# Kernel optimization log

Measured on AMD Instinct MI355X. Metric: run time of the kernel, lower is better.

## Reference

```python
import jax, jax.numpy as jnp
import numpy as np

B, C = 8192, 1000
T_KD = 20.0   # KL_divergence temperature
T_TH = 2.0    # Threshold_weights5 temperature
ALPHA = 0.8   # dynamic weight scale


def setup_inputs() -> dict:
    key = jax.random.key(0)
    ks = jax.random.split(key, 7)
    d = {f"outputs{i+1}": jax.random.normal(ks[i], (B, C), jnp.float32) for i in range(5)}
    d["out_s"] = jax.random.normal(ks[5], (B, C), jnp.float32)
    d["targets"] = jax.random.randint(ks[6], (B,), 0, C)
    return d


def _margin(o, targets):
    # per-sample: top1 - top2 if the target class holds the max logit, else 0
    top2 = jax.lax.top_k(o, 2)[0]                                   # [B, 2]
    tgt = jnp.take_along_axis(o, targets[:, None], axis=1)[:, 0]    # [B]
    return jnp.where(tgt == top2[:, 0], top2[:, 0] - top2[:, 1], jnp.zeros_like(tgt))


def reference(outputs1, outputs2, outputs3, outputs4, outputs5, out_s, targets):
    teachers = jnp.stack([outputs1, outputs2, outputs3, outputs4, outputs5], 0)  # [5,B,C]
    mimic = teachers.mean(0)                                                      # [B,C]
    all6 = jnp.concatenate([teachers, mimic[None]], axis=0)                       # [6,B,C]

    # Threshold_weights5: confidence margins -> softmax over the 6 sources
    margins = jax.vmap(lambda o: _margin(o, targets))(all6)        # [6,B]
    out_threshold = jax.nn.softmax(margins / T_TH, axis=0)         # [6,B]
    max_preds = teachers.max()                                     # scalar

    # Calculate_dynamic_weights for each source
    tgt_logits = jnp.take_along_axis(all6, targets[None, :, None], axis=2)[..., 0]  # [6,B]
    w2 = ALPHA * tgt_logits / max_preds                            # [6,B]
    w1 = 1.0 - w2                                                  # [6,B]

    # CE loss (shared across sources) and KD cross-entropy per source
    log_p_s = jax.nn.log_softmax(out_s, axis=1)
    CE = -jnp.take_along_axis(log_p_s, targets[:, None], axis=1)[:, 0]             # [B]
    log_p_sT = jax.nn.log_softmax(out_s / T_KD, axis=1)                            # [B,C]
    p_t = jax.nn.softmax(all6 / T_KD, axis=2)                                      # [6,B,C]
    KD = -jnp.sum(p_t * log_p_sT[None], axis=2) * (T_KD * T_KD)                    # [6,B]

    loss_src = w1 * CE[None, :] + w2 * KD                          # [6,B]
    return jnp.mean(jnp.sum(out_threshold * loss_src, axis=0))
```

## Files before the change

kernel.cpp:

```cpp
#include <hip/hip_runtime.h>
#include <math.h>

#define NROWS 8192
#define NCOLS 1000
#define TPB   256
#define WPB   4
#define NB    (NROWS / WPB)
#define NSLOT 64
#define NEGF  -1.0e30f


__device__ __forceinline__ unsigned encf(float x) {
    unsigned u = __float_as_uint(x);
    return (u & 0x80000000u) ? ~u : (u | 0x80000000u);
}
__device__ __forceinline__ float decf(unsigned e) {
    unsigned u = (e & 0x80000000u) ? (e ^ 0x80000000u) : ~e;
    return __uint_as_float(u);
}
__device__ __forceinline__ float pick4(const float* a, int k) {
    return k == 0 ? a[0] : (k == 1 ? a[1] : (k == 2 ? a[2] : a[3]));
}

__global__ __launch_bounds__(TPB, 4) void row_kernel(
    const float* __restrict__ p0, const float* __restrict__ p1,
    const float* __restrict__ p2, const float* __restrict__ p3,
    const float* __restrict__ p4, const float* __restrict__ p5,
    const int* __restrict__ targets,
    double* __restrict__ S1, double* __restrict__ S2, unsigned* __restrict__ MX)
{
    const int wave = threadIdx.x >> 6;
    const int l    = threadIdx.x & 63;
    const int row  = blockIdx.x * WPB + wave;

    const int tgt = targets[row];
    const int t4  = tgt >> 2;
    const int lt  = t4 & 63;
    const int qt  = t4 >> 6;
    const int kt  = tgt & 3;

    float m1[6], m2[6], zs[6], ds[6];
    #pragma unroll
    for (int s = 0; s < 6; ++s) { m1[s] = NEGF; m2[s] = NEGF; zs[s] = 0.f; ds[s] = 0.f; }
    float z1 = 0.f, z20 = 0.f;
    float sg[7];
    #pragma unroll
    for (int s = 0; s < 7; ++s) sg[s] = 0.f;

    #pragma unroll 2
    for (int q = 0; q < 4; ++q) {
        const int  c4 = l + (q << 6);
        const bool ok = (c4 < (NCOLS >> 2));
        const size_t base = (size_t)row * NCOLS + ((size_t)c4 << 2);

        float v[7][4];
        if (ok) {
            float4 x0 = *(const float4*)(p0 + base);
            float4 x1 = *(const float4*)(p1 + base);
            float4 x2 = *(const float4*)(p2 + base);
            float4 x3 = *(const float4*)(p3 + base);
            float4 x4 = *(const float4*)(p4 + base);
            float4 x5 = *(const float4*)(p5 + base);
            v[0][0]=x0.x; v[0][1]=x0.y; v[0][2]=x0.z; v[0][3]=x0.w;
            v[1][0]=x1.x; v[1][1]=x1.y; v[1][2]=x1.z; v[1][3]=x1.w;
            v[2][0]=x2.x; v[2][1]=x2.y; v[2][2]=x2.z; v[2][3]=x2.w;
            v[3][0]=x3.x; v[3][1]=x3.y; v[3][2]=x3.z; v[3][3]=x3.w;
            v[4][0]=x4.x; v[4][1]=x4.y; v[4][2]=x4.z; v[4][3]=x4.w;
            v[6][0]=x5.x; v[6][1]=x5.y; v[6][2]=x5.z; v[6][3]=x5.w;
            #pragma unroll
            for (int k = 0; k < 4; ++k)
                v[5][k] = (v[0][k] + v[1][k] + v[2][k] + v[3][k] + v[4][k]) * 0.2f;
        } else {
            #pragma unroll
            for (int s = 0; s < 7; ++s)
                #pragma unroll
                for (int k = 0; k < 4; ++k) v[s][k] = NEGF;
        }

        #pragma unroll
        for (int s = 0; s < 6; ++s) {
            float a = v[s][0], b = v[s][1], c = v[s][2], d = v[s][3];
            float hi1 = fmaxf(a, b), lo1 = fminf(a, b);
            float hi2 = fmaxf(c, d), lo2 = fminf(c, d);
            float q1 = fmaxf(hi1, hi2);
            float q2 = fmaxf(fminf(hi1, hi2), fmaxf(lo1, lo2));
            float nm1 = fmaxf(m1[s], q1);
            float nm2 = fmaxf(fminf(m1[s], q1), fmaxf(m2[s], q2));
            m1[s] = nm1; m2[s] = nm2;
            float zz = 0.f, dot = 0.f;
            #pragma unroll
            for (int k = 0; k < 4; ++k) {
                float e = __expf(v[s][k] * 0.05f);
                zz += e; dot += e * v[6][k];
            }
            zs[s] += zz; ds[s] += dot;
        }
        #pragma unroll
        for (int k = 0; k < 4; ++k) {
            z1  += __expf(v[6][k]);
            z20 += __expf(v[6][k] * 0.05f);
        }
        if (ok && q == qt && l == lt) {
            #pragma unroll
            for (int s = 0; s < 7; ++s) sg[s] = pick4(v[s], kt);
        }
    }

    #pragma unroll
    for (int xm = 1; xm < 64; xm <<= 1) {
        #pragma unroll
        for (int s = 0; s < 6; ++s) {
            float o1 = __shfl_xor(m1[s], xm);
            float o2 = __shfl_xor(m2[s], xm);
            float nm1 = fmaxf(m1[s], o1);
            float nm2 = fmaxf(fminf(m1[s], o1), fmaxf(m2[s], o2));
            m1[s] = nm1; m2[s] = nm2;
            zs[s] += __shfl_xor(zs[s], xm);
            ds[s] += __shfl_xor(ds[s], xm);
        }
        z1  += __shfl_xor(z1, xm);
        z20 += __shfl_xor(z20, xm);
    }
    float sgv[7];
    #pragma unroll
    for (int s = 0; s < 7; ++s) sgv[s] = __shfl(sg[s], lt);

    if (l == 0) {
        const float lse1  = logf(z1);
        const float lse20 = logf(z20);
        const float CE    = lse1 - sgv[6];

        float KD[6], mg[6];
        float mmax = 0.f;
        #pragma unroll
        for (int s = 0; s < 6; ++s) {
            KD[s] = 400.f * lse20 - 20.f * (ds[s] / zs[s]);
            mg[s] = (sgv[s] == m1[s]) ? (m1[s] - m2[s]) : 0.f;
            mmax  = fmaxf(mmax, mg[s]);
        }
        float es[6], se = 0.f;
        #pragma unroll
        for (int s = 0; s < 6; ++s) { es[s] = __expf((mg[s] - mmax) * 0.5f); se += es[s]; }

        double rS2 = 0.0;
        #pragma unroll
        for (int s = 0; s < 6; ++s)
            rS2 += (double)(es[s] / se) * (double)sgv[s] * (double)(KD[s] - CE);

        float tmax = fmaxf(fmaxf(fmaxf(m1[0], m1[1]), fmaxf(m1[2], m1[3])), m1[4]);
        atomicAdd(&S1[row & (NSLOT - 1)], (double)CE);
        atomicAdd(&S2[row & (NSLOT - 1)], rS2);
        atomicMax(&MX[row & (NSLOT - 1)], encf(tmax));
    }
}

__global__ void final_kernel(const double* __restrict__ S1, const double* __restrict__ S2,
                             const unsigned* __restrict__ MX, float* __restrict__ out)
{
    const int tid = threadIdx.x;
    double s1 = S1[tid], s2 = S2[tid];
    unsigned m = MX[tid];
    #pragma unroll
    for (int k = 32; k >= 1; k >>= 1) {
        s1 += __shfl_xor(s1, k);
        s2 += __shfl_xor(s2, k);
        unsigned om = __shfl_xor(m, k);
        m = (om > m) ? om : m;
    }
    if (tid == 0) {
        double maxp = (double)decf(m);
        out[0] = (float)((s1 + (0.8 / maxp) * s2) / (double)NROWS);
    }
}

extern "C" void kernel_launch(void* const* d_in, const int* in_sizes, int n_in,
                              void* d_out, int out_size, void* d_ws, size_t ws_size,
                              hipStream_t stream)
{
    const float* t1 = (const float*)d_in[0];
    const float* t2 = (const float*)d_in[1];
    const float* t3 = (const float*)d_in[2];
    const float* t4 = (const float*)d_in[3];
    const float* t5 = (const float*)d_in[4];
    const float* os = (const float*)d_in[5];
    const int* targets = (const int*)d_in[6];

    double*   S1 = (double*)d_ws;
    double*   S2 = S1 + NSLOT;
    unsigned* MX = (unsigned*)(S2 + NSLOT);

    hipMemsetAsync(d_ws, 0, NSLOT * (8 + 8 + 4), stream);
    row_kernel<<<NB, TPB, 0, stream>>>(t1, t2, t3, t4, t5, os, targets, S1, S2, MX);
    final_kernel<<<1, 64, 0, stream>>>(S1, S2, MX, (float*)d_out);
}
```

Before: 214.3 us.

## Software-pipeline row loads with inline asm double buffering and manual vmcnt waits

Replaces the compiler-scheduled column loop with explicit inline-asm global_load_dwordx4 batches into two register buffers. The next chunk's six loads are issued while the current chunk is processed, with s_waitcnt vmcnt gating each stage. The tail chunk clamps its address and masks padded lanes, so the bounds branch goes away. Launch bounds are relaxed from 4 to 3 waves per SIMD to fit the extra live registers, which trades occupancy for memory-level parallelism inside each wave.

```diff
diff --git a/kernel.cpp b/kernel.cpp
--- a/kernel.cpp
+++ b/kernel.cpp
@@ -9,6 +9,8 @@
 #define NSLOT 64
 #define NEGF  -1.0e30f
 
+typedef float f32x4 __attribute__((ext_vector_type(4)));
+
 
 __device__ __forceinline__ unsigned encf(float x) {
     unsigned u = __float_as_uint(x);
@@ -22,7 +24,78 @@
     return k == 0 ? a[0] : (k == 1 ? a[1] : (k == 2 ? a[2] : a[3]));
 }
 
-__global__ __launch_bounds__(TPB, 4) void row_kernel(
+#define LOAD6(X0,X1,X2,X3,X4,X5, A0,A1,A2,A3,A4,A5)                    \
+    asm volatile("global_load_dwordx4 %0, %6, off\n\t"                 \
+                 "global_load_dwordx4 %1, %7, off\n\t"                 \
+                 "global_load_dwordx4 %2, %8, off\n\t"                 \
+                 "global_load_dwordx4 %3, %9, off\n\t"                 \
+                 "global_load_dwordx4 %4, %10, off\n\t"                \
+                 "global_load_dwordx4 %5, %11, off"                    \
+                 : "=&v"(X0), "=&v"(X1), "=&v"(X2), "=&v"(X3), "=&v"(X4), "=&v"(X5) \
+                 : "v"(A0), "v"(A1), "v"(A2), "v"(A3), "v"(A4), "v"(A5) \
+                 : "memory")
+
+#define WAITVM(Nstr) do {                                              \
+    asm volatile("s_waitcnt vmcnt(" Nstr ")" ::: "memory");            \
+    __builtin_amdgcn_sched_barrier(0);                                 \
+} while (0)
+
+__device__ __forceinline__ void chunk_accum(
+    f32x4 X0, f32x4 X1, f32x4 X2, f32x4 X3, f32x4 X4, f32x4 X5,
+    int q, bool pad, int qt, int lt, int kt, int l,
+    float (&m1)[6], float (&m2)[6], float (&zs)[6], float (&ds)[6],
+    float &z1, float &z20, float (&sg)[7])
+{
+    float v[7][4];
+    #pragma unroll
+    for (int k = 0; k < 4; ++k) {
+        v[0][k] = X0[k]; v[1][k] = X1[k]; v[2][k] = X2[k];
+        v[3][k] = X3[k]; v[4][k] = X4[k]; v[6][k] = X5[k];
+    }
+    if (pad) {
+        #pragma unroll
+        for (int s = 0; s < 7; ++s)
+            #pragma unroll
+            for (int k = 0; k < 4; ++k) v[s][k] = NEGF;
+    }
+    #pragma unroll
+    for (int k = 0; k < 4; ++k)
+        v[5][k] = (v[0][k] + v[1][k] + v[2][k] + v[3][k] + v[4][k]) * 0.2f;
+    if (pad) {
+        #pragma unroll
+        for (int k = 0; k < 4; ++k) v[5][k] = NEGF;
+    }
+
+    #pragma unroll
+    for (int s = 0; s < 6; ++s) {
+        float a = v[s][0], b = v[s][1], c = v[s][2], d = v[s][3];
+        float hi1 = fmaxf(a, b), lo1 = fminf(a, b);
+        float hi2 = fmaxf(c, d), lo2 = fminf(c, d);
+        float q1 = fmaxf(hi1, hi2);
+        float q2 = fmaxf(fminf(hi1, hi2), fmaxf(lo1, lo2));
+        float nm1 = fmaxf(m1[s], q1);
+        float nm2 = fmaxf(fminf(m1[s], q1), fmaxf(m2[s], q2));
+        m1[s] = nm1; m2[s] = nm2;
+        float zz = 0.f, dot = 0.f;
+        #pragma unroll
+        for (int k = 0; k < 4; ++k) {
+            float e = __expf(v[s][k] * 0.05f);
+            zz += e; dot += e * v[6][k];
+        }
+        zs[s] += zz; ds[s] += dot;
+    }
+    #pragma unroll
+    for (int k = 0; k < 4; ++k) {
+        z1  += __expf(v[6][k]);
+        z20 += __expf(v[6][k] * 0.05f);
+    }
+    if (!pad && q == qt && l == lt) {
+        #pragma unroll
+        for (int s = 0; s < 7; ++s) sg[s] = pick4(v[s], kt);
+    }
+}
+
+__global__ __launch_bounds__(TPB, 3) void row_kernel(
     const float* __restrict__ p0, const float* __restrict__ p1,
     const float* __restrict__ p2, const float* __restrict__ p3,
     const float* __restrict__ p4, const float* __restrict__ p5,
@@ -32,12 +105,24 @@
     const int wave = threadIdx.x >> 6;
     const int l    = threadIdx.x & 63;
     const int row  = blockIdx.x * WPB + wave;
+    const size_t rbase = (size_t)row * NCOLS;
 
     const int tgt = targets[row];
     const int t4  = tgt >> 2;
     const int lt  = t4 & 63;
     const int qt  = t4 >> 6;
     const int kt  = tgt & 3;
+    __builtin_amdgcn_sched_barrier(0);
+
+    int c4t = l + 192; if (c4t > 249) c4t = 249;
+    const size_t off0 = rbase + ((size_t)l << 2);
+    const size_t off1 = off0 + 256;
+    const size_t off2 = off0 + 512;
+    const size_t offT = rbase + ((size_t)c4t << 2);
+
+    f32x4 X0,X1,X2,X3,X4,X5, Y0,Y1,Y2,Y3,Y4,Y5;
+    LOAD6(X0,X1,X2,X3,X4,X5, p0+off0, p1+off0, p2+off0, p3+off0, p4+off0, p5+off0);
+    LOAD6(Y0,Y1,Y2,Y3,Y4,Y5, p0+off1, p1+off1, p2+off1, p3+off1, p4+off1, p5+off1);
 
     float m1[6], m2[6], zs[6], ds[6];
     #pragma unroll
@@ -47,64 +132,19 @@
     #pragma unroll
     for (int s = 0; s < 7; ++s) sg[s] = 0.f;
 
-    #pragma unroll 2
-    for (int q = 0; q < 4; ++q) {
-        const int  c4 = l + (q << 6);
-        const bool ok = (c4 < (NCOLS >> 2));
-        const size_t base = (size_t)row * NCOLS + ((size_t)c4 << 2);
-
-        float v[7][4];
-        if (ok) {
-            float4 x0 = *(const float4*)(p0 + base);
-            float4 x1 = *(const float4*)(p1 + base);
-            float4 x2 = *(const float4*)(p2 + base);
-            float4 x3 = *(const float4*)(p3 + base);
-            float4 x4 = *(const float4*)(p4 + base);
-            float4 x5 = *(const float4*)(p5 + base);
-            v[0][0]=x0.x; v[0][1]=x0.y; v[0][2]=x0.z; v[0][3]=x0.w;
-            v[1][0]=x1.x; v[1][1]=x1.y; v[1][2]=x1.z; v[1][3]=x1.w;
-            v[2][0]=x2.x; v[2][1]=x2.y; v[2][2]=x2.z; v[2][3]=x2.w;
-            v[3][0]=x3.x; v[3][1]=x3.y; v[3][2]=x3.z; v[3][3]=x3.w;
-            v[4][0]=x4.x; v[4][1]=x4.y; v[4][2]=x4.z; v[4][3]=x4.w;
-            v[6][0]=x5.x; v[6][1]=x5.y; v[6][2]=x5.z; v[6][3]=x5.w;
-            #pragma unroll
-            for (int k = 0; k < 4; ++k)
-                v[5][k] = (v[0][k] + v[1][k] + v[2][k] + v[3][k] + v[4][k]) * 0.2f;
-        } else {
-            #pragma unroll
-            for (int s = 0; s < 7; ++s)
-                #pragma unroll
-                for (int k = 0; k < 4; ++k) v[s][k] = NEGF;
-        }
-
-        #pragma unroll
-        for (int s = 0; s < 6; ++s) {
-            float a = v[s][0], b = v[s][1], c = v[s][2], d = v[s][3];
-            float hi1 = fmaxf(a, b), lo1 = fminf(a, b);
-            float hi2 = fmaxf(c, d), lo2 = fminf(c, d);
-            float q1 = fmaxf(hi1, hi2);
-            float q2 = fmaxf(fminf(hi1, hi2), fmaxf(lo1, lo2));
-            float nm1 = fmaxf(m1[s], q1);
-            float nm2 = fmaxf(fminf(m1[s], q1), fmaxf(m2[s], q2));
-            m1[s] = nm1; m2[s] = nm2;
-            float zz = 0.f, dot = 0.f;
-            #pragma unroll
-            for (int k = 0; k < 4; ++k) {
-                float e = __expf(v[s][k] * 0.05f);
-                zz += e; dot += e * v[6][k];
-            }
-            zs[s] += zz; ds[s] += dot;
-        }
-        #pragma unroll
-        for (int k = 0; k < 4; ++k) {
-            z1  += __expf(v[6][k]);
-            z20 += __expf(v[6][k] * 0.05f);
-        }
-        if (ok && q == qt && l == lt) {
-            #pragma unroll
-            for (int s = 0; s < 7; ++s) sg[s] = pick4(v[s], kt);
-        }
-    }
+    WAITVM("6");
+    chunk_accum(X0,X1,X2,X3,X4,X5, 0, false, qt,lt,kt,l, m1,m2,zs,ds, z1,z20, sg);
+    LOAD6(X0,X1,X2,X3,X4,X5, p0+off2, p1+off2, p2+off2, p3+off2, p4+off2, p5+off2);
+
+    WAITVM("6");
+    chunk_accum(Y0,Y1,Y2,Y3,Y4,Y5, 1, false, qt,lt,kt,l, m1,m2,zs,ds, z1,z20, sg);
+    LOAD6(Y0,Y1,Y2,Y3,Y4,Y5, p0+offT, p1+offT, p2+offT, p3+offT, p4+offT, p5+offT);
+
+    WAITVM("6");
+    chunk_accum(X0,X1,X2,X3,X4,X5, 2, false, qt,lt,kt,l, m1,m2,zs,ds, z1,z20, sg);
+
+    WAITVM("0");
+    chunk_accum(Y0,Y1,Y2,Y3,Y4,Y5, 3, (l >= 58), qt,lt,kt,l, m1,m2,zs,ds, z1,z20, sg);
 
     #pragma unroll
     for (int xm = 1; xm < 64; xm <<= 1) {
```

Result: no change. 211.1 us (-1.5%).

## Split each row across two waves with a partial-merge kernel pair

Applied to the files above, without the earlier changes.

Each row is now processed by two wavefronts, each covering half of the 1000 columns. All twelve float4 loads are issued up front to raise memory-level parallelism. Per-half partial statistics (top-2, softmax sums, dot products, target gathers) go to a workspace buffer, and a new merge kernel combines them and does the per-row loss. This doubles the wave count and the in-flight loads. The cost is an extra launch, a workspace round-trip and a fallback path when the workspace is too small.

```diff
diff --git a/kernel.cpp b/kernel.cpp
--- a/kernel.cpp
+++ b/kernel.cpp
@@ -3,12 +3,11 @@
 
 #define NROWS 8192
 #define NCOLS 1000
-#define TPB   256
-#define WPB   4
-#define NB    (NROWS / WPB)
 #define NSLOT 64
 #define NEGF  -1.0e30f
-
+#define NHALF (NROWS * 2)
+#define NCOMP 33
+#define WS_NEEDED (1536u + (size_t)NCOMP * NHALF * 4u)
 
 __device__ __forceinline__ unsigned encf(float x) {
     unsigned u = __float_as_uint(x);
@@ -22,7 +21,198 @@
     return k == 0 ? a[0] : (k == 1 ? a[1] : (k == 2 ? a[2] : a[3]));
 }
 
-__global__ __launch_bounds__(TPB, 4) void row_kernel(
+__global__ __launch_bounds__(256) void partial_kernel(
+    const float* __restrict__ p0, const float* __restrict__ p1,
+    const float* __restrict__ p2, const float* __restrict__ p3,
+    const float* __restrict__ p4, const float* __restrict__ p5,
+    const int* __restrict__ targets, float* __restrict__ part)
+{
+    const int wid = blockIdx.x * 4 + (threadIdx.x >> 6);
+    const int l   = threadIdx.x & 63;
+    const int row = wid >> 1;
+    const int h   = wid & 1;
+    const size_t rbase = (size_t)row * NCOLS;
+
+    const int tgt = targets[row];
+    const int c4t = tgt >> 2;
+    const int ht  = (c4t >= 125) ? 1 : 0;
+    const int local = c4t - ht * 125;
+    const int qt  = (local >= 64) ? 1 : 0;
+    const int lt  = qt ? (local - 64) : local;
+    const int kt  = tgt & 3;
+    const bool own = (h == ht);
+
+    const int  c40 = h * 125 + l;
+    const bool ok1 = (l < 61);
+    const int  c41 = h * 125 + (ok1 ? (64 + l) : 124);
+    const size_t off0 = rbase + ((size_t)c40 << 2);
+    const size_t off1 = rbase + ((size_t)c41 << 2);
+
+    float4 A0 = *(const float4*)(p0 + off0), B0 = *(const float4*)(p0 + off1);
+    float4 A1 = *(const float4*)(p1 + off0), B1 = *(const float4*)(p1 + off1);
+    float4 A2 = *(const float4*)(p2 + off0), B2 = *(const float4*)(p2 + off1);
+    float4 A3 = *(const float4*)(p3 + off0), B3 = *(const float4*)(p3 + off1);
+    float4 A4 = *(const float4*)(p4 + off0), B4 = *(const float4*)(p4 + off1);
+    float4 A5 = *(const float4*)(p5 + off0), B5 = *(const float4*)(p5 + off1);
+
+    float m1[6], m2[6], zs[6], ds[6];
+    #pragma unroll
+    for (int s = 0; s < 6; ++s) { m1[s] = NEGF; m2[s] = NEGF; zs[s] = 0.f; ds[s] = 0.f; }
+    float z1 = 0.f, z20 = 0.f;
+    float sg[7];
+    #pragma unroll
+    for (int s = 0; s < 7; ++s) sg[s] = 0.f;
+
+    #pragma unroll
+    for (int q = 0; q < 2; ++q) {
+        float v[7][4];
+        if (q == 0) {
+            v[0][0]=A0.x; v[0][1]=A0.y; v[0][2]=A0.z; v[0][3]=A0.w;
+            v[1][0]=A1.x; v[1][1]=A1.y; v[1][2]=A1.z; v[1][3]=A1.w;
+            v[2][0]=A2.x; v[2][1]=A2.y; v[2][2]=A2.z; v[2][3]=A2.w;
+            v[3][0]=A3.x; v[3][1]=A3.y; v[3][2]=A3.z; v[3][3]=A3.w;
+            v[4][0]=A4.x; v[4][1]=A4.y; v[4][2]=A4.z; v[4][3]=A4.w;
+            v[6][0]=A5.x; v[6][1]=A5.y; v[6][2]=A5.z; v[6][3]=A5.w;
+        } else {
+            v[0][0]=B0.x; v[0][1]=B0.y; v[0][2]=B0.z; v[0][3]=B0.w;
+            v[1][0]=B1.x; v[1][1]=B1.y; v[1][2]=B1.z; v[1][3]=B1.w;
+            v[2][0]=B2.x; v[2][1]=B2.y; v[2][2]=B2.z; v[2][3]=B2.w;
+            v[3][0]=B3.x; v[3][1]=B3.y; v[3][2]=B3.z; v[3][3]=B3.w;
+            v[4][0]=B4.x; v[4][1]=B4.y; v[4][2]=B4.z; v[4][3]=B4.w;
+            v[6][0]=B5.x; v[6][1]=B5.y; v[6][2]=B5.z; v[6][3]=B5.w;
+        }
+        const bool pad = (q == 1) && !ok1;
+        if (pad) {
+            #pragma unroll
+            for (int s = 0; s < 7; ++s)
+                #pragma unroll
+                for (int k = 0; k < 4; ++k) v[s][k] = NEGF;
+        }
+        #pragma unroll
+        for (int k = 0; k < 4; ++k)
+            v[5][k] = (v[0][k] + v[1][k] + v[2][k] + v[3][k] + v[4][k]) * 0.2f;
+        if (pad) {
+            #pragma unroll
+            for (int k = 0; k < 4; ++k) v[5][k] = NEGF;
+        }
+
+        #pragma unroll
+        for (int s = 0; s < 6; ++s) {
+            float a = v[s][0], b = v[s][1], c = v[s][2], d = v[s][3];
+            float hi1 = fmaxf(a, b), lo1 = fminf(a, b);
+            float hi2 = fmaxf(c, d), lo2 = fminf(c, d);
+            float q1 = fmaxf(hi1, hi2);
+            float q2 = fmaxf(fminf(hi1, hi2), fmaxf(lo1, lo2));
+            float nm1 = fmaxf(m1[s], q1);
+            float nm2 = fmaxf(fminf(m1[s], q1), fmaxf(m2[s], q2));
+            m1[s] = nm1; m2[s] = nm2;
+            float zz = 0.f, dot = 0.f;
+            #pragma unroll
+            for (int k = 0; k < 4; ++k) {
+                float e = __expf(v[s][k] * 0.05f);
+                zz += e; dot += e * v[6][k];
+            }
+            zs[s] += zz; ds[s] += dot;
+        }
+        #pragma unroll
+        for (int k = 0; k < 4; ++k) {
+            z1  += __expf(v[6][k]);
+            z20 += __expf(v[6][k] * 0.05f);
+        }
+        if (own && q == qt && l == lt) {
+            #pragma unroll
+            for (int s = 0; s < 7; ++s) sg[s] = pick4(v[s], kt);
+        }
+    }
+
+    #pragma unroll
+    for (int xm = 1; xm < 64; xm <<= 1) {
+        #pragma unroll
+        for (int s = 0; s < 6; ++s) {
+            float o1 = __shfl_xor(m1[s], xm);
+            float o2 = __shfl_xor(m2[s], xm);
+            float nm1 = fmaxf(m1[s], o1);
+            float nm2 = fmaxf(fminf(m1[s], o1), fmaxf(m2[s], o2));
+            m1[s] = nm1; m2[s] = nm2;
+            zs[s] += __shfl_xor(zs[s], xm);
+            ds[s] += __shfl_xor(ds[s], xm);
+        }
+        z1  += __shfl_xor(z1, xm);
+        z20 += __shfl_xor(z20, xm);
+    }
+
+    if (l == 0) {
+        #pragma unroll
+        for (int s = 0; s < 6; ++s) {
+            part[(0  + s) * NHALF + wid] = m1[s];
+            part[(6  + s) * NHALF + wid] = m2[s];
+            part[(12 + s) * NHALF + wid] = zs[s];
+            part[(18 + s) * NHALF + wid] = ds[s];
+        }
+        part[24 * NHALF + wid] = z1;
+        part[25 * NHALF + wid] = z20;
+    }
+    if (own && l == lt) {
+        #pragma unroll
+        for (int s = 0; s < 7; ++s)
+            part[(26 + s) * NHALF + wid] = sg[s];
+    }
+}
+
+__global__ __launch_bounds__(256) void merge_kernel(
+    const float* __restrict__ part, const int* __restrict__ targets,
+    double* __restrict__ S1, double* __restrict__ S2, unsigned* __restrict__ MX)
+{
+    const int row = blockIdx.x * 256 + threadIdx.x;
+    const int w0 = row * 2, w1 = w0 + 1;
+
+    float m1[6], m2[6], zs[6], ds[6];
+    #pragma unroll
+    for (int s = 0; s < 6; ++s) {
+        float a1 = part[(0 + s) * NHALF + w0], b1 = part[(0 + s) * NHALF + w1];
+        float a2 = part[(6 + s) * NHALF + w0], b2 = part[(6 + s) * NHALF + w1];
+        m1[s] = fmaxf(a1, b1);
+        m2[s] = fmaxf(fminf(a1, b1), fmaxf(a2, b2));
+        zs[s] = part[(12 + s) * NHALF + w0] + part[(12 + s) * NHALF + w1];
+        ds[s] = part[(18 + s) * NHALF + w0] + part[(18 + s) * NHALF + w1];
+    }
+    const float z1  = part[24 * NHALF + w0] + part[24 * NHALF + w1];
+    const float z20 = part[25 * NHALF + w0] + part[25 * NHALF + w1];
+
+    const int tgt = targets[row];
+    const int wo  = ((tgt >> 2) >= 125) ? w1 : w0;
+    float sgv[7];
+    #pragma unroll
+    for (int s = 0; s < 7; ++s) sgv[s] = part[(26 + s) * NHALF + wo];
+
+    const float lse1  = logf(z1);
+    const float lse20 = logf(z20);
+    const float CE    = lse1 - sgv[6];
+
+    float KD[6], mg[6];
+    float mmax = 0.f;
+    #pragma unroll
+    for (int s = 0; s < 6; ++s) {
+        KD[s] = 400.f * lse20 - 20.f * (ds[s] / zs[s]);
+        mg[s] = (sgv[s] == m1[s]) ? (m1[s] - m2[s]) : 0.f;
+        mmax  = fmaxf(mmax, mg[s]);
+    }
+    float es[6], se = 0.f;
+    #pragma unroll
+    for (int s = 0; s < 6; ++s) { es[s] = __expf((mg[s] - mmax) * 0.5f); se += es[s]; }
+
+    double rS2 = 0.0;
+    #pragma unroll
+    for (int s = 0; s < 6; ++s)
+        rS2 += (double)(es[s] / se) * (double)sgv[s] * (double)(KD[s] - CE);
+
+    float tmax = fmaxf(fmaxf(fmaxf(m1[0], m1[1]), fmaxf(m1[2], m1[3])), m1[4]);
+    atomicAdd(&S1[row & (NSLOT - 1)], (double)CE);
+    atomicAdd(&S2[row & (NSLOT - 1)], rS2);
+    atomicMax(&MX[row & (NSLOT - 1)], encf(tmax));
+}
+
+__global__ __launch_bounds__(256, 4) void row_kernel_fb(
     const float* __restrict__ p0, const float* __restrict__ p1,
     const float* __restrict__ p2, const float* __restrict__ p3,
     const float* __restrict__ p4, const float* __restrict__ p5,
@@ -31,7 +221,7 @@
 {
     const int wave = threadIdx.x >> 6;
     const int l    = threadIdx.x & 63;
-    const int row  = blockIdx.x * WPB + wave;
+    const int row  = blockIdx.x * 4 + wave;
 
     const int tgt = targets[row];
     const int t4  = tgt >> 2;
@@ -185,11 +375,17 @@
     const float* os = (const float*)d_in[5];
     const int* targets = (const int*)d_in[6];
 
-    double*   S1 = (double*)d_ws;
-    double*   S2 = S1 + NSLOT;
-    unsigned* MX = (unsigned*)(S2 + NSLOT);
+    double*   S1   = (double*)d_ws;
+    double*   S2   = S1 + NSLOT;
+    unsigned* MX   = (unsigned*)(S2 + NSLOT);
+    float*    part = (float*)((char*)d_ws + 1536);
 
     hipMemsetAsync(d_ws, 0, NSLOT * (8 + 8 + 4), stream);
-    row_kernel<<<NB, TPB, 0, stream>>>(t1, t2, t3, t4, t5, os, targets, S1, S2, MX);
+    if (ws_size >= WS_NEEDED) {
+        partial_kernel<<<NHALF / 4, 256, 0, stream>>>(t1, t2, t3, t4, t5, os, targets, part);
+        merge_kernel<<<NROWS / 256, 256, 0, stream>>>(part, targets, S1, S2, MX);
+    } else {
+        row_kernel_fb<<<NROWS / 4, 256, 0, stream>>>(t1, t2, t3, t4, t5, os, targets, S1, S2, MX);
+    }
     final_kernel<<<1, 64, 0, stream>>>(S1, S2, MX, (float*)d_out);
 }
```

New measurement: 215.0 us. Within noise of the previous version (+0.3%).
